# Kernel optimization log

Measured on AMD Instinct MI355X. Metric: run time of the kernel, lower is better.

## Reference

```python
import jax, jax.numpy as jnp
import numpy as np

B = 2048
D = 256
C = 100000
SCALE = 30.0
MARGIN = 0.2
EPS = 1e-6


def setup_inputs() -> dict:
    key = jax.random.key(0)
    k1, k2, k3 = jax.random.split(key, 3)
    emb = jax.random.normal(k1, (B, D), dtype=jnp.float32)
    # speaker embeddings are typically L2-normalized; also keeps cosines in (-1,1)
    emb = emb / jnp.linalg.norm(emb, axis=1, keepdims=True)
    W = jax.random.normal(k2, (C, D), dtype=jnp.float32)
    targets = jax.random.randint(k3, (B,), 0, C, dtype=jnp.int64)
    return {"embedding": emb, "W": W, "targets": targets}


def reference(embedding, W, targets):
    # normalize classifier rows (F.normalize on weight, dim=1, eps=1e-12)
    Wn = W / jnp.maximum(jnp.linalg.norm(W, axis=1, keepdims=True), 1e-12)
    # [B, C] cosine logits, clamped as in the original
    cos = jnp.clip(embedding @ Wn.T, -1.0, 1.0)
    # per-sample target cosine -> margin-adjusted numerator
    tgt_cos = jnp.take_along_axis(cos, targets[:, None], axis=1)[:, 0]
    numerator = SCALE * jnp.cos(jnp.arccos(tgt_cos) + MARGIN)  # [B]
    # masked sum over non-target classes (replaces the python loop + cat)
    col = jnp.arange(C, dtype=targets.dtype)[None, :]
    not_target = (col != targets[:, None]).astype(cos.dtype)  # [B, C]
    excl_sum = jnp.sum(jnp.exp(SCALE * cos) * not_target, axis=1)  # [B]
    denominator = jnp.exp(numerator) + excl_sum
    loss = -jnp.mean(numerator - jnp.log(denominator + EPS))
    return loss
```

## Files before the change

kernel.cpp:

```cpp
#include <hip/hip_runtime.h>
#include <hip/hip_bf16.h>


static constexpr int Bn = 2048;
static constexpr int Dn = 256;
static constexpr int Cn = 100000;
static constexpr int NSLICE = 1564;
static constexpr int CPAD   = NSLICE * 64;
static constexpr float OOB_COLS = (float)(CPAD - Cn);
static constexpr int NT = Bn / 16;

#define SCALE_F 30.0f
#define MARGIN_F 0.2f
#define EPS_F 1e-6f

typedef __attribute__((ext_vector_type(8))) short bf16x8;
typedef __attribute__((ext_vector_type(4))) float f32x4;

__device__ __forceinline__ short f2bf_rne(float x) {
    union { float f; unsigned int u; } v; v.f = x;
    unsigned int r = v.u + 0x7fffu + ((v.u >> 16) & 1u);
    return (short)(r >> 16);
}

__global__ __launch_bounds__(256) void k_prep(const float* __restrict__ W,
                                              const float* __restrict__ emb,
                                              const int* __restrict__ tgt,
                                              short* __restrict__ embF,
                                              float* __restrict__ numv,
                                              float* __restrict__ etv) {
    const int blk = blockIdx.x;
    if (blk < 256) {
        const int t     = blk >> 1;
        const int chunk = (blk & 1) * 256 + threadIdx.x;
        const int ks    = chunk >> 6;
        const int lane  = chunk & 63;
        const int q     = lane >> 4;
        const int cr    = lane & 15;
        const float* src = emb + (size_t)(t * 16 + cr) * Dn + ks * 32 + q * 8;
        float4 x0 = *(const float4*)(src);
        float4 x1 = *(const float4*)(src + 4);
        bf16x8 o;
        o[0] = f2bf_rne(x0.x); o[1] = f2bf_rne(x0.y);
        o[2] = f2bf_rne(x0.z); o[3] = f2bf_rne(x0.w);
        o[4] = f2bf_rne(x1.x); o[5] = f2bf_rne(x1.y);
        o[6] = f2bf_rne(x1.z); o[7] = f2bf_rne(x1.w);
        *(bf16x8*)(embF + (size_t)((t * 8 + ks) * 64 + lane) * 8) = o;
    } else {
        const int b    = (blk - 256) * 4 + (threadIdx.x >> 6);
        const int lane = threadIdx.x & 63;
        const int t    = tgt[b];
        float4 x = *(const float4*)(W + (size_t)t * Dn + lane * 4);
        float4 e = *(const float4*)(emb + b * Dn + lane * 4);
        float dot = x.x * e.x + x.y * e.y + x.z * e.z + x.w * e.w;
        float ss  = x.x * x.x + x.y * x.y + x.z * x.z + x.w * x.w;
#pragma unroll
        for (int o = 1; o < 64; o <<= 1) {
            dot += __shfl_xor(dot, o);
            ss  += __shfl_xor(ss, o);
        }
        if (lane == 0) {
            float cosv = dot / fmaxf(sqrtf(ss), 1e-12f);
            cosv = fminf(fmaxf(cosv, -1.f), 1.f);
            const float num = SCALE_F * cosf(acosf(cosv) + MARGIN_F);
            numv[b] = num;
            etv[b]  = __expf(SCALE_F * cosv);
        }
    }
}

__global__ __launch_bounds__(64, 2) void k_main(const float* __restrict__ W,
                                                const short* __restrict__ embF,
                                                float* __restrict__ partial) {
    const int lane = threadIdx.x;
    const int q    = lane >> 4;
    const int cr   = lane & 15;
    const int sl   = blockIdx.x;
    const int cbase = sl * 64;

    bf16x8 afrag[4][8];
#pragma unroll
    for (int ct = 0; ct < 4; ++ct) {
        const int c = cbase + ct * 16 + cr;
        const float* wr = W + (size_t)c * Dn;
        float ss = 0.0f;
        if (c < Cn) {
#pragma unroll
            for (int ks = 0; ks < 8; ++ks) {
                float4 x0 = *(const float4*)(wr + ks * 32 + q * 8);
                float4 x1 = *(const float4*)(wr + ks * 32 + q * 8 + 4);
                ss += x0.x * x0.x + x0.y * x0.y + x0.z * x0.z + x0.w * x0.w;
                ss += x1.x * x1.x + x1.y * x1.y + x1.z * x1.z + x1.w * x1.w;
            }
        }
        ss += __shfl_xor(ss, 16);
        ss += __shfl_xor(ss, 32);
        const float rn = 1.0f / fmaxf(sqrtf(ss), 1e-12f);
#pragma unroll
        for (int ks = 0; ks < 8; ++ks) {
            bf16x8 a = {0, 0, 0, 0, 0, 0, 0, 0};
            if (c < Cn) {
                float4 x0 = *(const float4*)(wr + ks * 32 + q * 8);
                float4 x1 = *(const float4*)(wr + ks * 32 + q * 8 + 4);
                a[0] = f2bf_rne(x0.x * rn); a[1] = f2bf_rne(x0.y * rn);
                a[2] = f2bf_rne(x0.z * rn); a[3] = f2bf_rne(x0.w * rn);
                a[4] = f2bf_rne(x1.x * rn); a[5] = f2bf_rne(x1.y * rn);
                a[6] = f2bf_rne(x1.z * rn); a[7] = f2bf_rne(x1.w * rn);
            }
            afrag[ct][ks] = a;
        }
    }

    float* pout = partial + (size_t)sl * Bn;
    const bf16x8* bsrc = (const bf16x8*)embF;

    auto load_b = [&](bf16x8* bf, int t) {
        const bf16x8* p = bsrc + (size_t)t * 512 + lane;
#pragma unroll
        for (int ks = 0; ks < 8; ++ks) bf[ks] = p[ks * 64];
    };

    auto compute = [&](const bf16x8* bf, int t) {
        f32x4 a0 = {0.f, 0.f, 0.f, 0.f};
        f32x4 a1 = {0.f, 0.f, 0.f, 0.f};
        f32x4 a2 = {0.f, 0.f, 0.f, 0.f};
        f32x4 a3 = {0.f, 0.f, 0.f, 0.f};
#pragma unroll
        for (int ks = 0; ks < 8; ++ks) {
            a0 = __builtin_amdgcn_mfma_f32_16x16x32_bf16(afrag[0][ks], bf[ks], a0, 0, 0, 0);
            a1 = __builtin_amdgcn_mfma_f32_16x16x32_bf16(afrag[1][ks], bf[ks], a1, 0, 0, 0);
            a2 = __builtin_amdgcn_mfma_f32_16x16x32_bf16(afrag[2][ks], bf[ks], a2, 0, 0, 0);
            a3 = __builtin_amdgcn_mfma_f32_16x16x32_bf16(afrag[3][ks], bf[ks], a3, 0, 0, 0);
        }
        float s = 0.0f;
#pragma unroll
        for (int r = 0; r < 4; ++r) {
            s += __expf(SCALE_F * a0[r]);
            s += __expf(SCALE_F * a1[r]);
            s += __expf(SCALE_F * a2[r]);
            s += __expf(SCALE_F * a3[r]);
        }
        s += __shfl_xor(s, 16);
        s += __shfl_xor(s, 32);
        if (lane < 16) pout[t * 16 + cr] = s;
    };

    bf16x8 b0[8], b1[8];
    load_b(b0, 0);
    for (int t = 0; t < NT; t += 2) {
        load_b(b1, t + 1);
        compute(b0, t);
        load_b(b0, (t + 2) < NT ? (t + 2) : 0);
        compute(b1, t + 1);
    }
}

__global__ __launch_bounds__(256) void k_finish(const float* __restrict__ partial,
                                                const float* __restrict__ numv,
                                                const float* __restrict__ etv,
                                                float* __restrict__ out) {
    __shared__ float red[64];
    const int l  = threadIdx.x & 63;
    const int qq = threadIdx.x >> 6;
    const int b  = blockIdx.x * 64 + l;

    if (threadIdx.x < 64) red[threadIdx.x] = 0.0f;
    __syncthreads();

    const int s0 = qq * (NSLICE / 4);
    const int s1 = s0 + (NSLICE / 4);
    float acc = 0.0f;
    for (int s = s0; s < s1; ++s) acc += partial[(size_t)s * Bn + b];
    atomicAdd(&red[l], acc);
    __syncthreads();

    if (threadIdx.x < 64) {
        const float num  = numv[b];
        const float excl = red[l] - OOB_COLS - etv[b];
        const float denom = __expf(num) + excl;
        float term = num - logf(denom + EPS_F);
#pragma unroll
        for (int o = 1; o < 64; o <<= 1) term += __shfl_xor(term, o);
        if (l == 0) atomicAdd(out, -term / (float)Bn);
    }
}

extern "C" void kernel_launch(void* const* d_in, const int* in_sizes, int n_in,
                              void* d_out, int out_size, void* d_ws, size_t ws_size,
                              hipStream_t stream) {
    const float* emb = (const float*)d_in[0];
    const float* W   = (const float*)d_in[1];
    const int*   tgt = (const int*)d_in[2];
    float* out = (float*)d_out;

    char* ws = (char*)d_ws;
    short* embF    = (short*)ws;
    float* partial = (float*)(ws + (1 << 20));
    float* numv    = partial + (size_t)NSLICE * Bn;
    float* etv     = numv + Bn;

    hipMemsetAsync(out, 0, sizeof(float), stream);
    k_prep<<<768, 256, 0, stream>>>(W, emb, tgt, embF, numv, etv);
    k_main<<<NSLICE, 64, 0, stream>>>(W, embF, partial);
    k_finish<<<32, 256, 0, stream>>>(partial, numv, etv, out);
}
```

Baseline: 274.2 us.

## Halve class tile per block, apply row norm post-MFMA, reduce partials via atomic banks

Each block now handles 32 classes instead of 64, doubling the grid and raising the occupancy hint to 3 waves per SIMD. W rows are read once and converted to bf16 unnormalized, with the inverse norm folded into the exponent scale after the MFMA. The large per-slice partial buffer is replaced by 64 atomic accumulation banks, which shrinks the finish kernel's reads but adds atomic traffic and a memset. Because each block loads its embedding fragments once for half as many classes, embedding reuse per load is halved.

```diff
diff --git a/kernel.cpp b/kernel.cpp
--- a/kernel.cpp
+++ b/kernel.cpp
@@ -5,10 +5,11 @@
 static constexpr int Bn = 2048;
 static constexpr int Dn = 256;
 static constexpr int Cn = 100000;
-static constexpr int NSLICE = 1564;
-static constexpr int CPAD   = NSLICE * 64;
+static constexpr int NSLICE = 3128;
+static constexpr int CPAD   = NSLICE * 32;
 static constexpr float OOB_COLS = (float)(CPAD - Cn);
 static constexpr int NT = Bn / 16;
+static constexpr int NBANK = 64;
 
 #define SCALE_F 30.0f
 #define MARGIN_F 0.2f
@@ -69,18 +70,19 @@
     }
 }
 
-__global__ __launch_bounds__(64, 2) void k_main(const float* __restrict__ W,
+__global__ __launch_bounds__(64, 3) void k_main(const float* __restrict__ W,
                                                 const short* __restrict__ embF,
-                                                float* __restrict__ partial) {
+                                                float* __restrict__ banks) {
     const int lane = threadIdx.x;
     const int q    = lane >> 4;
     const int cr   = lane & 15;
     const int sl   = blockIdx.x;
-    const int cbase = sl * 64;
-
-    bf16x8 afrag[4][8];
-#pragma unroll
-    for (int ct = 0; ct < 4; ++ct) {
+    const int cbase = sl * 32;
+
+    bf16x8 afrag[2][8];
+    float  srn[2][4];
+#pragma unroll
+    for (int ct = 0; ct < 2; ++ct) {
         const int c = cbase + ct * 16 + cr;
         const float* wr = W + (size_t)c * Dn;
         float ss = 0.0f;
@@ -91,27 +93,26 @@
                 float4 x1 = *(const float4*)(wr + ks * 32 + q * 8 + 4);
                 ss += x0.x * x0.x + x0.y * x0.y + x0.z * x0.z + x0.w * x0.w;
                 ss += x1.x * x1.x + x1.y * x1.y + x1.z * x1.z + x1.w * x1.w;
+                bf16x8 a;
+                a[0] = f2bf_rne(x0.x); a[1] = f2bf_rne(x0.y);
+                a[2] = f2bf_rne(x0.z); a[3] = f2bf_rne(x0.w);
+                a[4] = f2bf_rne(x1.x); a[5] = f2bf_rne(x1.y);
+                a[6] = f2bf_rne(x1.z); a[7] = f2bf_rne(x1.w);
+                afrag[ct][ks] = a;
             }
+        } else {
+#pragma unroll
+            for (int ks = 0; ks < 8; ++ks) afrag[ct][ks] = bf16x8{0,0,0,0,0,0,0,0};
         }
         ss += __shfl_xor(ss, 16);
         ss += __shfl_xor(ss, 32);
         const float rn = 1.0f / fmaxf(sqrtf(ss), 1e-12f);
 #pragma unroll
-        for (int ks = 0; ks < 8; ++ks) {
-            bf16x8 a = {0, 0, 0, 0, 0, 0, 0, 0};
-            if (c < Cn) {
-                float4 x0 = *(const float4*)(wr + ks * 32 + q * 8);
-                float4 x1 = *(const float4*)(wr + ks * 32 + q * 8 + 4);
-                a[0] = f2bf_rne(x0.x * rn); a[1] = f2bf_rne(x0.y * rn);
-                a[2] = f2bf_rne(x0.z * rn); a[3] = f2bf_rne(x0.w * rn);
-                a[4] = f2bf_rne(x1.x * rn); a[5] = f2bf_rne(x1.y * rn);
-                a[6] = f2bf_rne(x1.z * rn); a[7] = f2bf_rne(x1.w * rn);
-            }
-            afrag[ct][ks] = a;
-        }
-    }
-
-    float* pout = partial + (size_t)sl * Bn;
+        for (int r = 0; r < 4; ++r)
+            srn[ct][r] = SCALE_F * __shfl(rn, q * 4 + r);
+    }
+
+    float* bout = banks + (size_t)(sl & (NBANK - 1)) * Bn;
     const bf16x8* bsrc = (const bf16x8*)embF;
 
     auto load_b = [&](bf16x8* bf, int t) {
@@ -123,26 +124,20 @@
     auto compute = [&](const bf16x8* bf, int t) {
         f32x4 a0 = {0.f, 0.f, 0.f, 0.f};
         f32x4 a1 = {0.f, 0.f, 0.f, 0.f};
-        f32x4 a2 = {0.f, 0.f, 0.f, 0.f};
-        f32x4 a3 = {0.f, 0.f, 0.f, 0.f};
 #pragma unroll
         for (int ks = 0; ks < 8; ++ks) {
             a0 = __builtin_amdgcn_mfma_f32_16x16x32_bf16(afrag[0][ks], bf[ks], a0, 0, 0, 0);
             a1 = __builtin_amdgcn_mfma_f32_16x16x32_bf16(afrag[1][ks], bf[ks], a1, 0, 0, 0);
-            a2 = __builtin_amdgcn_mfma_f32_16x16x32_bf16(afrag[2][ks], bf[ks], a2, 0, 0, 0);
-            a3 = __builtin_amdgcn_mfma_f32_16x16x32_bf16(afrag[3][ks], bf[ks], a3, 0, 0, 0);
         }
         float s = 0.0f;
 #pragma unroll
         for (int r = 0; r < 4; ++r) {
-            s += __expf(SCALE_F * a0[r]);
-            s += __expf(SCALE_F * a1[r]);
-            s += __expf(SCALE_F * a2[r]);
-            s += __expf(SCALE_F * a3[r]);
+            s += __expf(a0[r] * srn[0][r]);
+            s += __expf(a1[r] * srn[1][r]);
         }
         s += __shfl_xor(s, 16);
         s += __shfl_xor(s, 32);
-        if (lane < 16) pout[t * 16 + cr] = s;
+        if (lane < 16) atomicAdd(&bout[t * 16 + cr], s);
     };
 
     bf16x8 b0[8], b1[8];
@@ -155,7 +150,7 @@
     }
 }
 
-__global__ __launch_bounds__(256) void k_finish(const float* __restrict__ partial,
+__global__ __launch_bounds__(256) void k_finish(const float* __restrict__ banks,
                                                 const float* __restrict__ numv,
                                                 const float* __restrict__ etv,
                                                 float* __restrict__ out) {
@@ -167,10 +162,10 @@
     if (threadIdx.x < 64) red[threadIdx.x] = 0.0f;
     __syncthreads();
 
-    const int s0 = qq * (NSLICE / 4);
-    const int s1 = s0 + (NSLICE / 4);
     float acc = 0.0f;
-    for (int s = s0; s < s1; ++s) acc += partial[(size_t)s * Bn + b];
+#pragma unroll
+    for (int k = 0; k < NBANK / 4; ++k)
+        acc += banks[(size_t)(qq * (NBANK / 4) + k) * Bn + b];
     atomicAdd(&red[l], acc);
     __syncthreads();
 
@@ -194,13 +189,14 @@
     float* out = (float*)d_out;
 
     char* ws = (char*)d_ws;
-    short* embF    = (short*)ws;
-    float* partial = (float*)(ws + (1 << 20));
-    float* numv    = partial + (size_t)NSLICE * Bn;
-    float* etv     = numv + Bn;
+    short* embF  = (short*)ws;
+    float* banks = (float*)(ws + (1 << 20));
+    float* numv  = banks + (size_t)NBANK * Bn;
+    float* etv   = numv + Bn;
 
     hipMemsetAsync(out, 0, sizeof(float), stream);
+    hipMemsetAsync(banks, 0, (size_t)NBANK * Bn * sizeof(float), stream);
     k_prep<<<768, 256, 0, stream>>>(W, emb, tgt, embF, numv, etv);
-    k_main<<<NSLICE, 64, 0, stream>>>(W, embF, partial);
-    k_finish<<<32, 256, 0, stream>>>(partial, numv, etv, out);
-}
+    k_main<<<NSLICE, 64, 0, stream>>>(W, embF, banks);
+    k_finish<<<32, 256, 0, stream>>>(banks, numv, etv, out);
+}
```

Result: slower. 318.1 us (+16.0%).
